# Kernel optimization log

Measured on AMD Instinct MI355X. Metric: run time of the kernel, lower is better.

## Reference

```python
import jax, jax.numpy as jnp
import numpy as np


def setup_inputs() -> dict:
    key = jax.random.key(0)
    k1, k2 = jax.random.split(key)
    z = jax.random.normal(k1, (16, 256, 32, 32), dtype=jnp.float32)
    emb = jax.random.normal(k2, (8192, 256), dtype=jnp.float32)
    return {"z": z, "emb": emb}


def reference(z, emb):
    B, C, H, W = z.shape
    # [B,C,H,W] -> [B*H*W, C], distances in fp32 for precision
    z_f = jnp.transpose(z, (0, 2, 3, 1)).reshape(-1, C).astype(jnp.float32)
    e = emb.astype(jnp.float32)
    # squared-distance expansion: ||z||^2 - 2 z.e + ||e||^2  -> [N, K]
    d = (
        jnp.sum(z_f * z_f, axis=1, keepdims=True)
        - 2.0 * (z_f @ e.T)
        + jnp.sum(e * e, axis=1)[None, :]
    )
    idx = jnp.argmin(d, axis=1)  # [N]
    out = emb[idx].astype(z.dtype)  # codebook gather
    return jnp.transpose(out.reshape(B, H, W, C), (0, 3, 1, 2))
```

## Files before the change

### kernel.cpp

```cpp
#include <hip/hip_runtime.h>
#include <stdint.h>

#define NB   16
#define CD   256
#define HW   1024
#define NQ   16384
#define KCN  8192

typedef unsigned long long u64;
typedef unsigned short     u16;
using f32x4  = __attribute__((ext_vector_type(4))) float;
using bf16x8 = __attribute__((ext_vector_type(8))) __bf16;

#define ZTB_OFF  0
#define EMBB_OFF 8388608
#define EH_OFF   12582912
#define CAND_OFF 12615680

static __device__ __forceinline__ void gl_lds16(const void* g, void* l) {
  __builtin_amdgcn_global_load_lds(
      (const __attribute__((address_space(1))) void*)g,
      (__attribute__((address_space(3))) void*)l, 16, 0, 0);
}

static __device__ __forceinline__ unsigned bf16r(float x) {
  unsigned u = __float_as_uint(x);
  return (u + 0x7fffu + ((u >> 16) & 1u)) >> 16;
}

static __device__ __forceinline__ u64 umin64(u64 a, u64 b) { return a < b ? a : b; }
static __device__ __forceinline__ u64 umax64(u64 a, u64 b) { return a < b ? b : a; }

__global__ __launch_bounds__(256) void k_prep(const float* __restrict__ z,
                                              const float* __restrict__ emb,
                                              u16* __restrict__ zTb,
                                              u16* __restrict__ embB,
                                              float* __restrict__ eH) {
  const int bx = (int)blockIdx.x;
  if (bx < 1024) {
    __shared__ float tile[64][65];
    const int b   = bx >> 6;
    const int hwT = (bx >> 2) & 15;
    const int cT  = bx & 3;
    const int tx  = threadIdx.x & 63;
    const int ty  = threadIdx.x >> 6;
    const float* src = z + (size_t)(b * CD + cT * 64) * HW + hwT * 64;
#pragma unroll
    for (int i = 0; i < 16; ++i) {
      const int c_l = ty + 4 * i;
      tile[c_l][tx] = src[(size_t)c_l * HW + tx];
    }
    __syncthreads();
    const size_t dbase = (size_t)(b * HW + hwT * 64) * CD + cT * 64;
#pragma unroll
    for (int i = 0; i < 16; ++i) {
      const int hw_l = ty + 4 * i;
      zTb[dbase + (size_t)hw_l * CD + tx] = (u16)bf16r(tile[tx][hw_l]);
    }
  } else {
    const int wave = (bx - 1024) * 4 + ((int)threadIdx.x >> 6);
    const int lane = threadIdx.x & 63;
#pragma unroll
    for (int it = 0; it < 8; ++it) {
      const int row = wave * 8 + it;
      const float4 v = *(const float4*)(emb + (size_t)row * CD + lane * 4);
      uint2 pk;
      pk.x = bf16r(v.x) | (bf16r(v.y) << 16);
      pk.y = bf16r(v.z) | (bf16r(v.w) << 16);
      *(uint2*)(embB + (size_t)row * CD + lane * 4) = pk;
      float s = v.x * v.x + v.y * v.y + v.z * v.z + v.w * v.w;
#pragma unroll
      for (int off = 32; off; off >>= 1) s += __shfl_xor(s, off, 64);
      if (lane == 0) eH[row] = 0.5f * s + 1024.0f;
    }
  }
}


#define WAITV(N) asm volatile("s_waitcnt vmcnt(" #N ")" ::: "memory")
#define MEMFENCE() asm volatile("" ::: "memory")

__global__ __launch_bounds__(256, 2) void k_argmin(const u16* __restrict__ zTb,
                                                   const u16* __restrict__ embB,
                                                   const float* __restrict__ eH,
                                                   u64* __restrict__ cand) {
  __shared__ __align__(16) u16 Bs[3][128 * 64];

  const int tid  = (int)threadIdx.x;
  const int w    = tid >> 6;
  const int lane = tid & 63;
  const int l15  = lane & 15, quad = lane >> 4;
  const int q0    = (int)(blockIdx.x >> 3) * 128;
  const int split = (int)(blockIdx.x & 7);

  bf16x8 Af[2][4][2];
  {
    const char* aB = (const char*)zTb
                   + ((size_t)(q0 + w * 32 + l15) * CD + quad * 8) * 2;
#pragma unroll
    for (int i = 0; i < 2; ++i)
#pragma unroll
      for (int kc = 0; kc < 4; ++kc)
#pragma unroll
        for (int ks = 0; ks < 2; ++ks)
          Af[i][kc][ks] = *(const bf16x8*)(aB + i * 8192 + kc * 128 + ks * 64);
  }
  MEMFENCE();

  const char* bS = (const char*)embB + (size_t)split * (1024 * 512)
                 + (size_t)(w * 32 + (lane >> 3)) * 512
                 + (size_t)(((lane & 7) ^ (lane >> 3)) * 16);
  const int ldsW = w * 4096 + lane * 16;

#define STAGEP(P_, NT_, KC_)                                                   \
  do {                                                                         \
    const char* _s = bS + (NT_) * 65536 + (KC_) * 128;                         \
    char* _d = (char*)(P_) + ldsW;                                             \
    gl_lds16(_s,         _d);                                                  \
    gl_lds16(_s + 4096,  _d + 1024);                                           \
    gl_lds16(_s + 8192,  _d + 2048);                                           \
    gl_lds16(_s + 12288, _d + 3072);                                           \
  } while (0)

  const int bR0 = l15 * 128 + ((quad ^ (l15 & 7)) * 16);
  const int bR1 = bR0 ^ 64;

  f32x4 acc[2][8];
  float b1[8][2], b2[8][2];
  const float FMAX = __uint_as_float(0x7F7FFFFFu);
#pragma unroll
  for (int s = 0; s < 8; ++s) { b1[s][0] = b1[s][1] = FMAX; b2[s][0] = b2[s][1] = FMAX; }

  char* p0 = (char*)Bs[0];
  char* p1 = (char*)Bs[1];
  char* p2 = (char*)Bs[2];

  STAGEP(p0, 0, 0); MEMFENCE();
  STAGEP(p1, 0, 1); MEMFENCE();

#define MFMA_P(P_, KC_)                                                        \
  do {                                                                         \
    const char* _b = (const char*)(P_);                                        \
    _Pragma("unroll")                                                          \
    for (int ks = 0; ks < 2; ++ks) {                                           \
      bf16x8 bfr[8];                                                           \
      const int _o = ks ? bR1 : bR0;                                           \
      _Pragma("unroll")                                                        \
      for (int j = 0; j < 8; ++j)                                              \
        bfr[j] = *(const bf16x8*)(_b + j * 2048 + _o);                         \
      __builtin_amdgcn_s_setprio(1);                                           \
      _Pragma("unroll")                                                        \
      for (int i = 0; i < 2; ++i)                                              \
        _Pragma("unroll")                                                      \
        for (int j = 0; j < 8; ++j)                                            \
          acc[i][j] = __builtin_amdgcn_mfma_f32_16x16x32_bf16(                 \
              Af[i][KC_][ks], bfr[j], acc[i][j], 0, 0, 0);                     \
      __builtin_amdgcn_s_setprio(0);                                           \
    }                                                                          \
  } while (0)

#define EPILOGUE(NT_)                                                          \
  do {                                                                         \
    _Pragma("unroll")                                                          \
    for (int i = 0; i < 2; ++i)                                                \
      _Pragma("unroll")                                                        \
      for (int r = 0; r < 4; ++r) {                                            \
        const int s = i * 4 + r;                                               \
        float kq[8];                                                           \
        _Pragma("unroll")                                                      \
        for (int j = 0; j < 8; ++j)                                            \
          kq[j] = __uint_as_float(                                             \
              (__float_as_uint(eh[j] - acc[i][j][r]) & ~63u)                   \
              | (unsigned)((NT_) * 8 + j));                                    \
        _Pragma("unroll")                                                      \
        for (int h = 0; h < 2; ++h) {                                          \
          const float k0 = kq[4 * h], k1 = kq[4 * h + 1];                      \
          const float k2 = kq[4 * h + 2], k3 = kq[4 * h + 3];                  \
          const float lo01 = fminf(k0, k1), hi01 = fmaxf(k0, k1);              \
          const float lo23 = fminf(k2, k3), hi23 = fmaxf(k2, k3);              \
          const float best = fminf(lo01, lo23);                                \
          const float sec  = fminf(fmaxf(lo01, lo23), fminf(hi01, hi23));      \
          b2[s][h] = fminf(fmaxf(best, b1[s][h]), fminf(sec, b2[s][h]));       \
          b1[s][h] = fminf(best, b1[s][h]);                                    \
        }                                                                      \
      }                                                                        \
  } while (0)

  float eh[8];

  for (int nt = 0; nt < 7; ++nt) {
    const int n0 = split * 1024 + nt * 128;
#pragma unroll
    for (int i = 0; i < 2; ++i)
#pragma unroll
      for (int j = 0; j < 8; ++j) acc[i][j] = f32x4{0.f, 0.f, 0.f, 0.f};

    WAITV(4); __builtin_amdgcn_s_barrier(); MEMFENCE();
    STAGEP(p2, nt, 2); MEMFENCE();
#pragma unroll
    for (int j = 0; j < 8; ++j) eh[j] = eH[n0 + j * 16 + l15];
    MEMFENCE();
    MFMA_P(p0, 0);

    WAITV(12); __builtin_amdgcn_s_barrier(); MEMFENCE();
    STAGEP(p0, nt, 3); MEMFENCE();
    MFMA_P(p1, 1);

    WAITV(12); __builtin_amdgcn_s_barrier(); MEMFENCE();
    STAGEP(p1, nt + 1, 0); MEMFENCE();
    MFMA_P(p2, 2);

    WAITV(4); __builtin_amdgcn_s_barrier(); MEMFENCE();
    STAGEP(p2, nt + 1, 1); MEMFENCE();
    MFMA_P(p0, 3);

    EPILOGUE(nt);

    char* tmp = p0; p0 = p1; p1 = p2; p2 = tmp;
  }

  {
    const int n0 = split * 1024 + 7 * 128;
#pragma unroll
    for (int i = 0; i < 2; ++i)
#pragma unroll
      for (int j = 0; j < 8; ++j) acc[i][j] = f32x4{0.f, 0.f, 0.f, 0.f};

    WAITV(4); __builtin_amdgcn_s_barrier(); MEMFENCE();
    STAGEP(p2, 7, 2); MEMFENCE();
#pragma unroll
    for (int j = 0; j < 8; ++j) eh[j] = eH[n0 + j * 16 + l15];
    MEMFENCE();
    MFMA_P(p0, 0);

    WAITV(12); __builtin_amdgcn_s_barrier(); MEMFENCE();
    STAGEP(p0, 7, 3); MEMFENCE();
    MFMA_P(p1, 1);

    WAITV(12); __builtin_amdgcn_s_barrier(); MEMFENCE();
    MFMA_P(p2, 2);

    WAITV(0); __builtin_amdgcn_s_barrier(); MEMFENCE();
    MFMA_P(p0, 3);

    EPILOGUE(7);
  }
#undef STAGEP
#undef MFMA_P
#undef EPILOGUE

#pragma unroll
  for (int s = 0; s < 8; ++s) {
#pragma unroll
    for (int h = 0; h < 2; ++h) {
      u64 x1 = ((u64)__float_as_uint(b1[s][h]) << 32) | (unsigned)l15;
      u64 x2 = ((u64)__float_as_uint(b2[s][h]) << 32) | (unsigned)l15;
#pragma unroll
      for (int off = 1; off < 16; off <<= 1) {
        const u64 o1 = __shfl_xor(x1, off, 64);
        const u64 o2 = __shfl_xor(x2, off, 64);
        const u64 lo = umin64(x1, o1);
        const u64 hi = umax64(x1, o1);
        x1 = lo;
        x2 = umin64(hi, umin64(x2, o2));
      }
      if (l15 == 0) {
        const int i = s >> 2, r = s & 3;
        const int q = q0 + w * 32 + i * 16 + quad * 4 + r;
        const unsigned kb1 = (unsigned)(x1 >> 32), kb2 = (unsigned)(x2 >> 32);
        const int n1 = split * 1024 + (int)((kb1 >> 3) & 7) * 128
                       + (int)(kb1 & 7) * 16 + (int)(x1 & 15);
        const int n2 = split * 1024 + (int)((kb2 >> 3) & 7) * 128
                       + (int)(kb2 & 7) * 16 + (int)(x2 & 15);
        cand[(size_t)q * 32 + split * 4 + h * 2 + 0] = ((u64)kb1 << 32) | (unsigned)n1;
        cand[(size_t)q * 32 + split * 4 + h * 2 + 1] = ((u64)kb2 << 32) | (unsigned)n2;
      }
    }
  }
}

__global__ __launch_bounds__(1024) void k_pick_out(const float* __restrict__ z,
                                                   const float* __restrict__ emb,
                                                   const u64* __restrict__ cand,
                                                   float* __restrict__ out) {
  __shared__ float zs[64][256];
  const int t    = (int)threadIdx.x;
  const int lane = t & 63;
  const int wv   = t >> 6;
  const int l15  = t & 15;
  const int g    = t >> 4;
  const int q0b  = (int)blockIdx.x * 64;
  const int b    = q0b >> 10, hw0 = q0b & 1023;

  {
    const float* zb = z + ((size_t)(b * CD + wv * 16)) * HW + hw0;
    const int sw = lane & 31;
#pragma unroll
    for (int i = 0; i < 16; ++i)
      zs[lane][(wv * 16 + i) ^ sw] = zb[(size_t)i * HW + lane];
  }
  __syncthreads();

  const int q = q0b + g;
  const u64* cp = cand + (size_t)q * 32 + l15 * 2;
  const u64 v0 = cp[0], v1 = cp[1];
  u64 s0 = umin64(v0, v1), s1 = umax64(v0, v1), s2 = ~0ull, s3 = ~0ull;
#pragma unroll
  for (int off = 1; off < 16; off <<= 1) {
    const u64 b0 = __shfl_xor(s0, off, 64);
    const u64 b1 = __shfl_xor(s1, off, 64);
    const u64 b2 = __shfl_xor(s2, off, 64);
    const u64 b3 = __shfl_xor(s3, off, 64);
    const u64 c0 = umin64(s0, b0);
    const u64 c1 = umin64(umin64(s1, b1), umax64(s0, b0));
    const u64 c2 = umin64(umin64(s2, b2),
                          umin64(umax64(s1, b0), umax64(s0, b1)));
    const u64 c3 = umin64(umin64(umin64(s3, b3), umax64(s2, b0)),
                          umin64(umax64(s0, b2), umax64(s1, b1)));
    s0 = c0; s1 = c1; s2 = c2; s3 = c3;
  }
  const u64 sel[4] = {s0, s1, s2, s3};

  const int swq = g & 31;
  float zq[16];
#pragma unroll
  for (int j = 0; j < 16; ++j) zq[j] = zs[g][(j * 16 + l15) ^ swq];

  double bd = 1e300;
  int bi = 0x7fffffff;
  float keep[16];
#pragma unroll
  for (int j = 0; j < 16; ++j) keep[j] = 0.f;
#pragma unroll
  for (int c4 = 0; c4 < 4; ++c4) {
    const int idx = (int)(unsigned)(sel[c4] & 0xffffffffull);
    const float* er = emb + (size_t)idx * CD;
    float ev[16];
#pragma unroll
    for (int j = 0; j < 16; ++j) ev[j] = er[j * 16 + l15];
    double s = 0.0;
#pragma unroll
    for (int j = 0; j < 16; ++j) {
      const double d = (double)zq[j] - (double)ev[j];
      s += d * d;
    }
#pragma unroll
    for (int off = 1; off < 16; off <<= 1) s += __shfl_xor(s, off, 64);
    const bool better = (s < bd) || (s == bd && idx < bi);
    if (better) {
      bd = s; bi = idx;
#pragma unroll
      for (int j = 0; j < 16; ++j) keep[j] = ev[j];
    }
  }

  __syncthreads();
#pragma unroll
  for (int j = 0; j < 16; ++j) zs[g][(j * 16 + l15) ^ swq] = keep[j];
  __syncthreads();
  {
    float* ob = out + ((size_t)(b * CD + wv * 16)) * HW + hw0;
    const int sw = lane & 31;
#pragma unroll
    for (int i = 0; i < 16; ++i)
      ob[(size_t)i * HW + lane] = zs[lane][(wv * 16 + i) ^ sw];
  }
}

extern "C" void kernel_launch(void* const* d_in, const int* in_sizes, int n_in,
                              void* d_out, int out_size, void* d_ws, size_t ws_size,
                              hipStream_t stream) {
  const float* z   = (const float*)d_in[0];
  const float* emb = (const float*)d_in[1];
  float* out = (float*)d_out;

  char* ws = (char*)d_ws;
  u16*   zTb  = (u16*)(ws + ZTB_OFF);
  u16*   embB = (u16*)(ws + EMBB_OFF);
  float* eH   = (float*)(ws + EH_OFF);
  u64*   cand = (u64*)(ws + CAND_OFF);

  k_prep<<<1280, 256, 0, stream>>>(z, emb, zTb, embB, eH);
  k_argmin<<<1024, 256, 0, stream>>>(zTb, embB, eH, cand);
  k_pick_out<<<256, 1024, 0, stream>>>(z, emb, cand, out);
}
```

Measured before the change: 175.0 us.

## Replace LDS-staged codebook pipeline with direct register loads per wave

The k_argmin kernel drops its triple-buffered LDS staging (global_load_lds, barriers, vmcnt waits). Each wave now loads codebook B fragments straight from global memory into registers, double-buffered across 16-column tiles. Waves are repartitioned so each one owns 64 queries and half of the split's 512 codes, which removes all cross-wave synchronisation. In exchange, B fragments are no longer shared through LDS, so each code row is fetched by two waves and global/L2 traffic roughly doubles. The epilogue tracks a single candidate per tile with a 5-bit tile tag, and the top-2 output layout per half is kept.

```diff
diff --git a/kernel.cpp b/kernel.cpp
--- a/kernel.cpp
+++ b/kernel.cpp
@@ -16,12 +16,6 @@
 #define EMBB_OFF 8388608
 #define EH_OFF   12582912
 #define CAND_OFF 12615680
-
-static __device__ __forceinline__ void gl_lds16(const void* g, void* l) {
-  __builtin_amdgcn_global_load_lds(
-      (const __attribute__((address_space(1))) void*)g,
-      (__attribute__((address_space(3))) void*)l, 16, 0, 0);
-}
 
 static __device__ __forceinline__ unsigned bf16r(float x) {
   unsigned u = __float_as_uint(x);
@@ -76,205 +70,118 @@
   }
 }
 
-
-#define WAITV(N) asm volatile("s_waitcnt vmcnt(" #N ")" ::: "memory")
-#define MEMFENCE() asm volatile("" ::: "memory")
-
 __global__ __launch_bounds__(256, 2) void k_argmin(const u16* __restrict__ zTb,
                                                    const u16* __restrict__ embB,
                                                    const float* __restrict__ eH,
                                                    u64* __restrict__ cand) {
-  __shared__ __align__(16) u16 Bs[3][128 * 64];
-
   const int tid  = (int)threadIdx.x;
   const int w    = tid >> 6;
   const int lane = tid & 63;
   const int l15  = lane & 15, quad = lane >> 4;
   const int q0    = (int)(blockIdx.x >> 3) * 128;
   const int split = (int)(blockIdx.x & 7);
-
-  bf16x8 Af[2][4][2];
+  const int wq0 = (w & 1) * 64;
+  const int nh  = w >> 1;
+
+  bf16x8 Af[4][4][2];
   {
-    const char* aB = (const char*)zTb
-                   + ((size_t)(q0 + w * 32 + l15) * CD + quad * 8) * 2;
-#pragma unroll
-    for (int i = 0; i < 2; ++i)
+    const char* aB = (const char*)zTb + (size_t)(q0 + wq0 + l15) * 512 + quad * 16;
+#pragma unroll
+    for (int i = 0; i < 4; ++i)
 #pragma unroll
       for (int kc = 0; kc < 4; ++kc)
 #pragma unroll
         for (int ks = 0; ks < 2; ++ks)
           Af[i][kc][ks] = *(const bf16x8*)(aB + i * 8192 + kc * 128 + ks * 64);
   }
-  MEMFENCE();
-
-  const char* bS = (const char*)embB + (size_t)split * (1024 * 512)
-                 + (size_t)(w * 32 + (lane >> 3)) * 512
-                 + (size_t)(((lane & 7) ^ (lane >> 3)) * 16);
-  const int ldsW = w * 4096 + lane * 16;
-
-#define STAGEP(P_, NT_, KC_)                                                   \
+
+  const char* bP = (const char*)embB
+                 + (size_t)(split * 1024 + nh * 512 + l15) * 512 + quad * 16;
+  const float* ehP = eH + split * 1024 + nh * 512 + l15;
+
+  f32x4 acc[4];
+  float b1[16], b2[16];
+  const float FMAX = __uint_as_float(0x7F7FFFFFu);
+#pragma unroll
+  for (int s = 0; s < 16; ++s) { b1[s] = FMAX; b2[s] = FMAX; }
+
+#define LOADT(BUF, EHV, T)                                                     \
   do {                                                                         \
-    const char* _s = bS + (NT_) * 65536 + (KC_) * 128;                         \
-    char* _d = (char*)(P_) + ldsW;                                             \
-    gl_lds16(_s,         _d);                                                  \
-    gl_lds16(_s + 4096,  _d + 1024);                                           \
-    gl_lds16(_s + 8192,  _d + 2048);                                           \
-    gl_lds16(_s + 12288, _d + 3072);                                           \
+    const char* _p = bP + (size_t)(T) * 8192;                                  \
+    BUF[0] = *(const bf16x8*)(_p + 0);                                         \
+    BUF[1] = *(const bf16x8*)(_p + 64);                                        \
+    BUF[2] = *(const bf16x8*)(_p + 128);                                       \
+    BUF[3] = *(const bf16x8*)(_p + 192);                                       \
+    BUF[4] = *(const bf16x8*)(_p + 256);                                       \
+    BUF[5] = *(const bf16x8*)(_p + 320);                                       \
+    BUF[6] = *(const bf16x8*)(_p + 384);                                       \
+    BUF[7] = *(const bf16x8*)(_p + 448);                                       \
+    EHV = ehP[(T) * 16];                                                       \
   } while (0)
 
-  const int bR0 = l15 * 128 + ((quad ^ (l15 & 7)) * 16);
-  const int bR1 = bR0 ^ 64;
-
-  f32x4 acc[2][8];
-  float b1[8][2], b2[8][2];
-  const float FMAX = __uint_as_float(0x7F7FFFFFu);
-#pragma unroll
-  for (int s = 0; s < 8; ++s) { b1[s][0] = b1[s][1] = FMAX; b2[s][0] = b2[s][1] = FMAX; }
-
-  char* p0 = (char*)Bs[0];
-  char* p1 = (char*)Bs[1];
-  char* p2 = (char*)Bs[2];
-
-  STAGEP(p0, 0, 0); MEMFENCE();
-  STAGEP(p1, 0, 1); MEMFENCE();
-
-#define MFMA_P(P_, KC_)                                                        \
-  do {                                                                         \
-    const char* _b = (const char*)(P_);                                        \
-    _Pragma("unroll")                                                          \
-    for (int ks = 0; ks < 2; ++ks) {                                           \
-      bf16x8 bfr[8];                                                           \
-      const int _o = ks ? bR1 : bR0;                                           \
-      _Pragma("unroll")                                                        \
-      for (int j = 0; j < 8; ++j)                                              \
-        bfr[j] = *(const bf16x8*)(_b + j * 2048 + _o);                         \
-      __builtin_amdgcn_s_setprio(1);                                           \
-      _Pragma("unroll")                                                        \
-      for (int i = 0; i < 2; ++i)                                              \
-        _Pragma("unroll")                                                      \
-        for (int j = 0; j < 8; ++j)                                            \
-          acc[i][j] = __builtin_amdgcn_mfma_f32_16x16x32_bf16(                 \
-              Af[i][KC_][ks], bfr[j], acc[i][j], 0, 0, 0);                     \
-      __builtin_amdgcn_s_setprio(0);                                           \
-    }                                                                          \
-  } while (0)
-
-#define EPILOGUE(NT_)                                                          \
+#define MFMA_EPI(BUF, EHV, T)                                                  \
   do {                                                                         \
     _Pragma("unroll")                                                          \
-    for (int i = 0; i < 2; ++i)                                                \
+    for (int i = 0; i < 4; ++i) acc[i] = f32x4{0.f, 0.f, 0.f, 0.f};            \
+    _Pragma("unroll")                                                          \
+    for (int f = 0; f < 8; ++f)                                                \
+      _Pragma("unroll")                                                        \
+      for (int i = 0; i < 4; ++i)                                              \
+        acc[i] = __builtin_amdgcn_mfma_f32_16x16x32_bf16(                      \
+            Af[i][f >> 1][f & 1], BUF[f], acc[i], 0, 0, 0);                    \
+    _Pragma("unroll")                                                          \
+    for (int i = 0; i < 4; ++i)                                                \
       _Pragma("unroll")                                                        \
       for (int r = 0; r < 4; ++r) {                                            \
         const int s = i * 4 + r;                                               \
-        float kq[8];                                                           \
-        _Pragma("unroll")                                                      \
-        for (int j = 0; j < 8; ++j)                                            \
-          kq[j] = __uint_as_float(                                             \
-              (__float_as_uint(eh[j] - acc[i][j][r]) & ~63u)                   \
-              | (unsigned)((NT_) * 8 + j));                                    \
-        _Pragma("unroll")                                                      \
-        for (int h = 0; h < 2; ++h) {                                          \
-          const float k0 = kq[4 * h], k1 = kq[4 * h + 1];                      \
-          const float k2 = kq[4 * h + 2], k3 = kq[4 * h + 3];                  \
-          const float lo01 = fminf(k0, k1), hi01 = fmaxf(k0, k1);              \
-          const float lo23 = fminf(k2, k3), hi23 = fmaxf(k2, k3);              \
-          const float best = fminf(lo01, lo23);                                \
-          const float sec  = fminf(fmaxf(lo01, lo23), fminf(hi01, hi23));      \
-          b2[s][h] = fminf(fmaxf(best, b1[s][h]), fminf(sec, b2[s][h]));       \
-          b1[s][h] = fminf(best, b1[s][h]);                                    \
-        }                                                                      \
+        const unsigned kb = (__float_as_uint((EHV) - acc[i][r]) & ~31u)        \
+                            | (unsigned)(T);                                   \
+        const float k = __uint_as_float(kb);                                   \
+        b2[s] = fminf(fmaxf(k, b1[s]), b2[s]);                                 \
+        b1[s] = fminf(k, b1[s]);                                               \
       }                                                                        \
   } while (0)
 
-  float eh[8];
-
-  for (int nt = 0; nt < 7; ++nt) {
-    const int n0 = split * 1024 + nt * 128;
-#pragma unroll
-    for (int i = 0; i < 2; ++i)
-#pragma unroll
-      for (int j = 0; j < 8; ++j) acc[i][j] = f32x4{0.f, 0.f, 0.f, 0.f};
-
-    WAITV(4); __builtin_amdgcn_s_barrier(); MEMFENCE();
-    STAGEP(p2, nt, 2); MEMFENCE();
-#pragma unroll
-    for (int j = 0; j < 8; ++j) eh[j] = eH[n0 + j * 16 + l15];
-    MEMFENCE();
-    MFMA_P(p0, 0);
-
-    WAITV(12); __builtin_amdgcn_s_barrier(); MEMFENCE();
-    STAGEP(p0, nt, 3); MEMFENCE();
-    MFMA_P(p1, 1);
-
-    WAITV(12); __builtin_amdgcn_s_barrier(); MEMFENCE();
-    STAGEP(p1, nt + 1, 0); MEMFENCE();
-    MFMA_P(p2, 2);
-
-    WAITV(4); __builtin_amdgcn_s_barrier(); MEMFENCE();
-    STAGEP(p2, nt + 1, 1); MEMFENCE();
-    MFMA_P(p0, 3);
-
-    EPILOGUE(nt);
-
-    char* tmp = p0; p0 = p1; p1 = p2; p2 = tmp;
-  }
-
-  {
-    const int n0 = split * 1024 + 7 * 128;
-#pragma unroll
-    for (int i = 0; i < 2; ++i)
-#pragma unroll
-      for (int j = 0; j < 8; ++j) acc[i][j] = f32x4{0.f, 0.f, 0.f, 0.f};
-
-    WAITV(4); __builtin_amdgcn_s_barrier(); MEMFENCE();
-    STAGEP(p2, 7, 2); MEMFENCE();
-#pragma unroll
-    for (int j = 0; j < 8; ++j) eh[j] = eH[n0 + j * 16 + l15];
-    MEMFENCE();
-    MFMA_P(p0, 0);
-
-    WAITV(12); __builtin_amdgcn_s_barrier(); MEMFENCE();
-    STAGEP(p0, 7, 3); MEMFENCE();
-    MFMA_P(p1, 1);
-
-    WAITV(12); __builtin_amdgcn_s_barrier(); MEMFENCE();
-    MFMA_P(p2, 2);
-
-    WAITV(0); __builtin_amdgcn_s_barrier(); MEMFENCE();
-    MFMA_P(p0, 3);
-
-    EPILOGUE(7);
-  }
-#undef STAGEP
-#undef MFMA_P
-#undef EPILOGUE
-
-#pragma unroll
-  for (int s = 0; s < 8; ++s) {
-#pragma unroll
-    for (int h = 0; h < 2; ++h) {
-      u64 x1 = ((u64)__float_as_uint(b1[s][h]) << 32) | (unsigned)l15;
-      u64 x2 = ((u64)__float_as_uint(b2[s][h]) << 32) | (unsigned)l15;
-#pragma unroll
-      for (int off = 1; off < 16; off <<= 1) {
-        const u64 o1 = __shfl_xor(x1, off, 64);
-        const u64 o2 = __shfl_xor(x2, off, 64);
-        const u64 lo = umin64(x1, o1);
-        const u64 hi = umax64(x1, o1);
-        x1 = lo;
-        x2 = umin64(hi, umin64(x2, o2));
-      }
-      if (l15 == 0) {
-        const int i = s >> 2, r = s & 3;
-        const int q = q0 + w * 32 + i * 16 + quad * 4 + r;
-        const unsigned kb1 = (unsigned)(x1 >> 32), kb2 = (unsigned)(x2 >> 32);
-        const int n1 = split * 1024 + (int)((kb1 >> 3) & 7) * 128
-                       + (int)(kb1 & 7) * 16 + (int)(x1 & 15);
-        const int n2 = split * 1024 + (int)((kb2 >> 3) & 7) * 128
-                       + (int)(kb2 & 7) * 16 + (int)(x2 & 15);
-        cand[(size_t)q * 32 + split * 4 + h * 2 + 0] = ((u64)kb1 << 32) | (unsigned)n1;
-        cand[(size_t)q * 32 + split * 4 + h * 2 + 1] = ((u64)kb2 << 32) | (unsigned)n2;
-      }
+  bf16x8 bA[8], bB[8];
+  float ehA, ehB;
+
+  LOADT(bA, ehA, 0);
+  for (int tp = 0; tp < 15; ++tp) {
+    const int t = 2 * tp;
+    LOADT(bB, ehB, t + 1);
+    MFMA_EPI(bA, ehA, t);
+    LOADT(bA, ehA, t + 2);
+    MFMA_EPI(bB, ehB, t + 1);
+  }
+  LOADT(bB, ehB, 31);
+  MFMA_EPI(bA, ehA, 30);
+  MFMA_EPI(bB, ehB, 31);
+#undef LOADT
+#undef MFMA_EPI
+
+#pragma unroll
+  for (int s = 0; s < 16; ++s) {
+    u64 x1 = ((u64)__float_as_uint(b1[s]) << 32) | (unsigned)l15;
+    u64 x2 = ((u64)__float_as_uint(b2[s]) << 32) | (unsigned)l15;
+#pragma unroll
+    for (int off = 1; off < 16; off <<= 1) {
+      const u64 o1 = __shfl_xor(x1, off, 64);
+      const u64 o2 = __shfl_xor(x2, off, 64);
+      const u64 lo = umin64(x1, o1);
+      const u64 hi = umax64(x1, o1);
+      x1 = lo;
+      x2 = umin64(hi, umin64(x2, o2));
+    }
+    if (l15 == 0) {
+      const int i = s >> 2, r = s & 3;
+      const int q = q0 + wq0 + i * 16 + quad * 4 + r;
+      const unsigned kb1 = (unsigned)(x1 >> 32), kb2 = (unsigned)(x2 >> 32);
+      const int n1 = split * 1024 + nh * 512 + (int)(kb1 & 31u) * 16
+                     + (int)(x1 & 15);
+      const int n2 = split * 1024 + nh * 512 + (int)(kb2 & 31u) * 16
+                     + (int)(x2 & 15);
+      cand[(size_t)q * 32 + split * 4 + nh * 2 + 0] = ((u64)kb1 << 32) | (unsigned)n1;
+      cand[(size_t)q * 32 + split * 4 + nh * 2 + 1] = ((u64)kb2 << 32) | (unsigned)n2;
     }
   }
 }
```

After: 231.0 us. 32.0% more time.
